# Kernel tuning notes

Hardware: AMD Instinct MI355X
Metric: run time of the kernel (lower is better)

The kernel has to match this reference:

```python
import jax, jax.numpy as jnp
import numpy as np

NUM_HEADS = 12
HEAD_DIM = 64
LOGIT_SCALE_MAX = 4.605170185988092  # log(1/0.01), open_clip default
EPS = 1e-12  # F.normalize eps


def setup_inputs() -> dict:
    key = jax.random.key(0)
    ks = jax.random.split(key, 8)
    N, L, C = 2, 2048, 768
    return {
        "x": jax.random.normal(ks[0], (N, L, C), dtype=jnp.float32),
        "in_proj_w": jax.random.normal(ks[1], (3 * C, C), dtype=jnp.float32) * 0.02,
        "in_proj_b": jax.random.normal(ks[2], (3 * C,), dtype=jnp.float32) * 0.02,
        "logit_scale": jax.random.normal(ks[3], (NUM_HEADS, 1, 1), dtype=jnp.float32),
        "learned_scale": jnp.ones((NUM_HEADS,), dtype=jnp.float32),
        "out_proj_w": jax.random.normal(ks[4], (C, C), dtype=jnp.float32) * 0.02,
        "out_proj_b": jax.random.normal(ks[5], (C,), dtype=jnp.float32) * 0.02,
        "attn_mask": jnp.zeros((L, L), dtype=jnp.float32),
    }


def _l2norm(t):
    # F.normalize(dim=-1): x / max(||x||, eps)
    n = jnp.linalg.norm(t, axis=-1, keepdims=True)
    return t / jnp.maximum(n, EPS)


def reference(x, in_proj_w, in_proj_b, logit_scale, learned_scale,
              out_proj_w, out_proj_b, attn_mask):
    N, L, C = x.shape
    H, D = NUM_HEADS, HEAD_DIM
    # packed QKV projection: [N, L, 3C]
    qkv = jnp.einsum("nlc,fc->nlf", x, in_proj_w) + in_proj_b
    q, k, v = jnp.split(qkv, 3, axis=-1)
    # [N, L, C] -> [N, H, L, D]
    to_heads = lambda t: t.reshape(N, L, H, D).transpose(0, 2, 1, 3)
    q, k, v = to_heads(q), to_heads(k), to_heads(v)
    # cosine attention with clamped exp logit scale per head
    attn = jnp.einsum("nhld,nhmd->nhlm", _l2norm(q), _l2norm(k))
    ls = jnp.exp(jnp.minimum(logit_scale, LOGIT_SCALE_MAX))  # [H,1,1]
    attn = attn * ls[None]  # broadcast over [N,H,L,L]
    attn = attn + attn_mask  # additive mask [L,L]
    attn = jax.nn.softmax(attn, axis=-1)
    out = jnp.einsum("nhlm,nhmd->nhld", attn, v)
    # learned per-head output scale
    out = out * learned_scale[None, :, None, None]
    # [N,H,L,D] -> [N,L,C]
    out = out.transpose(0, 2, 1, 3).reshape(N, L, C)
    out = jnp.einsum("nlc,fc->nlf", out, out_proj_w) + out_proj_b
    return out
```

## Files before the change

### kernel.cpp

```cpp
#include <hip/hip_runtime.h>
#include <math.h>

#define NB   2
#define SEQ  2048
#define CH   768
#define NH   12
#define HD   64
#define F3   2304
#define LSMAX 4.605170185988092f
#define LOG2E 1.4426950408889634f

typedef _Float16 f16;
typedef __attribute__((ext_vector_type(8))) _Float16 f16x8;
typedef __attribute__((ext_vector_type(4))) _Float16 f16x4;
typedef __attribute__((ext_vector_type(2))) _Float16 f16x2;
typedef __attribute__((ext_vector_type(4))) float f32x4;
typedef __attribute__((ext_vector_type(16))) float f32x16;

typedef __attribute__((address_space(3))) void lds_void;
typedef __attribute__((address_space(1))) const void gbl_cvoid;

#define QSZ   3145728
#define OATT  (3 * QSZ)
#define XHOFF 12582912
#define W1OFF 15728640
#define W2OFF 17498112
#define FLAGO 18087936

#define VCH   2048
#define VPLN  131072

#define GP2  72

#define KOFF(s, b) (((s) * 2 + (b)) * 2048)
#define VOFF(s, b) (8192 + ((s) * 2 + (b)) * 2304)

__global__ __launch_bounds__(256) void cvt_f16(const float* __restrict__ X,
                                               const float* __restrict__ W1,
                                               const float* __restrict__ W2,
                                               const float* __restrict__ M,
                                               f16* __restrict__ Xh,
                                               f16* __restrict__ W1h,
                                               f16* __restrict__ W2h,
                                               int* __restrict__ flag)
{
    int tid = blockIdx.x * 256 + threadIdx.x;
    if (blockIdx.y == 3) {
        if (tid < 1048576) {
            float4 v = ((const float4*)M)[tid];
            bool nz = (v.x != 0.f) || (v.y != 0.f) || (v.z != 0.f) || (v.w != 0.f);
            if (__any(nz) && (threadIdx.x & 63) == 0) atomicOr(flag, 1);
        }
        return;
    }
    const float* src; f16* dst; int n4;
    switch (blockIdx.y) {
        case 0:  src = X;  dst = Xh;  n4 = 786432;  break;
        case 1:  src = W1; dst = W1h; n4 = 442368;  break;
        default: src = W2; dst = W2h; n4 = 147456;  break;
    }
    if (tid < n4) {
        float4 v = ((const float4*)src)[tid];
        f16x4 o = {(f16)v.x, (f16)v.y, (f16)v.z, (f16)v.w};
        ((f16x4*)dst)[tid] = o;
    }
}

__global__ __launch_bounds__(256, 4) void qkv_gemm(const f16* __restrict__ Xh,
                                                   const f16* __restrict__ Wh,
                                                   const float* __restrict__ bias,
                                                   const float* __restrict__ logit_scale,
                                                   f16* __restrict__ qkv16)
{
    __shared__ f16 As[2][128 * 32];
    __shared__ f16 Bs[2][128 * 32];
    const int t    = threadIdx.x;
    const int w    = t >> 6;
    const int lane = t & 63;
    const int quad = lane >> 4;
    const int sub  = lane & 15;
    const int wm   = w & 1, wn = w >> 1;
    const int f0   = blockIdx.x * 128;
    const int m0   = blockIdx.y * 128;

    const int s0 = t, s1 = 256 + t;
    const int r0 = s0 >> 2, cb0 = ((s0 & 3) ^ (r0 & 3)) * 8;
    const int r1 = s1 >> 2, cb1 = ((s1 & 3) ^ (r1 & 3)) * 8;
    const f16* ga0 = Xh + (size_t)(m0 + r0) * CH + cb0;
    const f16* ga1 = Xh + (size_t)(m0 + r1) * CH + cb1;
    const f16* gb0 = Wh + (size_t)(f0 + r0) * CH + cb0;
    const f16* gb1 = Wh + (size_t)(f0 + r1) * CH + cb1;

    f32x4 acc[4][4];
#pragma unroll
    for (int i = 0; i < 4; ++i)
#pragma unroll
        for (int j = 0; j < 4; ++j) acc[i][j] = (f32x4){0.f, 0.f, 0.f, 0.f};

    const int pch = (quad ^ (sub & 3)) * 8;

    __builtin_amdgcn_global_load_lds((gbl_cvoid*)(ga0), (lds_void*)&As[0][s0 * 8], 16, 0, 0);
    __builtin_amdgcn_global_load_lds((gbl_cvoid*)(ga1), (lds_void*)&As[0][s1 * 8], 16, 0, 0);
    __builtin_amdgcn_global_load_lds((gbl_cvoid*)(gb0), (lds_void*)&Bs[0][s0 * 8], 16, 0, 0);
    __builtin_amdgcn_global_load_lds((gbl_cvoid*)(gb1), (lds_void*)&Bs[0][s1 * 8], 16, 0, 0);
    __syncthreads();

    for (int k0 = 0; k0 < CH; k0 += 32) {
        const int cur = (k0 >> 5) & 1, nxt = cur ^ 1;
        if (k0 + 32 < CH) {
            __builtin_amdgcn_global_load_lds((gbl_cvoid*)(ga0 + k0 + 32), (lds_void*)&As[nxt][s0 * 8], 16, 0, 0);
            __builtin_amdgcn_global_load_lds((gbl_cvoid*)(ga1 + k0 + 32), (lds_void*)&As[nxt][s1 * 8], 16, 0, 0);
            __builtin_amdgcn_global_load_lds((gbl_cvoid*)(gb0 + k0 + 32), (lds_void*)&Bs[nxt][s0 * 8], 16, 0, 0);
            __builtin_amdgcn_global_load_lds((gbl_cvoid*)(gb1 + k0 + 32), (lds_void*)&Bs[nxt][s1 * 8], 16, 0, 0);
        }
        f16x8 af[4], bf[4];
#pragma unroll
        for (int i = 0; i < 4; ++i) {
            af[i] = *(const f16x8*)&As[cur][(wm * 64 + i * 16 + sub) * 32 + pch];
            bf[i] = *(const f16x8*)&Bs[cur][(wn * 64 + i * 16 + sub) * 32 + pch];
        }
#pragma unroll
        for (int i = 0; i < 4; ++i)
#pragma unroll
            for (int j = 0; j < 4; ++j)
                acc[i][j] = __builtin_amdgcn_mfma_f32_16x16x32_f16(af[i], bf[j], acc[i][j], 0, 0, 0);
        __syncthreads();
    }

    const int t3 = f0 / CH;
    const int h  = ((f0 + wn * 64) % CH) >> 6;
    float bb[4];
#pragma unroll
    for (int j = 0; j < 4; ++j) bb[j] = bias[f0 + wn * 64 + j * 16 + sub];

    if (t3 == 2) {
        f16* vdst = qkv16 + (size_t)2 * QSZ;
#pragma unroll
        for (int i = 0; i < 4; ++i) {
            int mb = m0 + wm * 64 + i * 16 + quad * 4;
            int nn = mb >> 11, l0 = mb & 2047;
            f16* pl = vdst + (size_t)(nn * NH + h) * VPLN + (l0 >> 5) * VCH + (l0 & 31);
#pragma unroll
            for (int j = 0; j < 4; ++j) {
                f16x4 vv;
#pragma unroll
                for (int r = 0; r < 4; ++r) vv[r] = (f16)(acc[i][j][r] + bb[j]);
                *(f16x4*)(pl + (j * 16 + sub) * 32) = vv;
            }
        }
        return;
    }

    f16* dst = qkv16 + (size_t)t3 * QSZ;
    float lsv = (t3 == 0) ? __expf(fminf(logit_scale[h], LSMAX)) * LOG2E : 1.0f;
#pragma unroll
    for (int i = 0; i < 4; ++i) {
#pragma unroll
        for (int r = 0; r < 4; ++r) {
            int m = m0 + wm * 64 + i * 16 + quad * 4 + r;
            int n = m >> 11, l = m & 2047;
            float v[4];
#pragma unroll
            for (int j = 0; j < 4; ++j) v[j] = acc[i][j][r] + bb[j];
            float ss = v[0] * v[0] + v[1] * v[1] + v[2] * v[2] + v[3] * v[3];
#pragma unroll
            for (int mk = 1; mk < 16; mk <<= 1) ss += __shfl_xor(ss, mk, 64);
            float scale = 1.0f / fmaxf(sqrtf(ss), 1e-12f);
            if (t3 == 0) scale *= lsv;
            f16* drow = dst + (((size_t)n * NH + h) * SEQ + l) * HD;
#pragma unroll
            for (int j = 0; j < 4; ++j)
                drow[j * 16 + sub] = (f16)(v[j] * scale);
        }
    }
}

union V8 { f16x4 h[2]; f16x8 v; };
union U8 { int i[4]; f16x8 v; };

__device__ __forceinline__ void compute_chunk_lds(
    const f16* Kr, const f16* Vr, int rsw, int h2,
    const f16x8& qf0, const f16x8& qf1, const f16x8& qf2, const f16x8& qf3,
    int cc, bool has_mask, const float* __restrict__ Mg,
    f32x16& o0, f32x16& o1, float& m_run, float& l_acc)
{
    const f16x2 one2 = {(f16)1.f, (f16)1.f};
    f16x8 kf0 = *(const f16x8*)(Kr + ((8 * h2 + 0)  ^ rsw));
    f16x8 kf1 = *(const f16x8*)(Kr + ((8 * h2 + 16) ^ rsw));
    f16x8 kf2 = *(const f16x8*)(Kr + ((8 * h2 + 32) ^ rsw));
    f16x8 kf3 = *(const f16x8*)(Kr + ((8 * h2 + 48) ^ rsw));
    f32x16 sA = {};
    sA = __builtin_amdgcn_mfma_f32_32x32x16_f16(kf0, qf0, sA, 0, 0, 0);
    sA = __builtin_amdgcn_mfma_f32_32x32x16_f16(kf1, qf1, sA, 0, 0, 0);
    sA = __builtin_amdgcn_mfma_f32_32x32x16_f16(kf2, qf2, sA, 0, 0, 0);
    sA = __builtin_amdgcn_mfma_f32_32x32x16_f16(kf3, qf3, sA, 0, 0, 0);
    V8 va, vb, vc, vd;
    va.h[0] = *(const f16x4*)(Vr + 0);
    va.h[1] = *(const f16x4*)(Vr + 8);
    vb.h[0] = *(const f16x4*)(Vr + 16);
    vb.h[1] = *(const f16x4*)(Vr + 24);
    vc.h[0] = *(const f16x4*)(Vr + 1152 + 0);
    vc.h[1] = *(const f16x4*)(Vr + 1152 + 8);
    vd.h[0] = *(const f16x4*)(Vr + 1152 + 16);
    vd.h[1] = *(const f16x4*)(Vr + 1152 + 24);

    if (has_mask) {
#pragma unroll
        for (int rr = 0; rr < 16; ++rr) {
            int kk = cc * 32 + (rr & 3) + 8 * (rr >> 2) + 4 * h2;
            sA[rr] += LOG2E * Mg[kk];
        }
    }
    float mloc = sA[0];
#pragma unroll
    for (int rr = 1; rr < 16; ++rr) mloc = fmaxf(mloc, sA[rr]);
    float mfull = fmaxf(mloc, __shfl_xor(mloc, 32, 64));
    if (__any(mfull > m_run)) {
        float mnew = fmaxf(m_run, mfull);
        float al = exp2f(m_run - mnew);
        m_run = mnew;
        l_acc *= al;
#pragma unroll
        for (int rr = 0; rr < 16; ++rr) { o0[rr] *= al; o1[rr] *= al; }
    }
#pragma unroll
    for (int rr = 0; rr < 16; ++rr) sA[rr] = exp2f(sA[rr] - m_run);
#define PK(a, b) ({ f16x2 _t = {(f16)(a), (f16)(b)}; __builtin_bit_cast(int, _t); })
    U8 u0, u1;
    u0.i[0] = PK(sA[0], sA[1]);   u0.i[1] = PK(sA[2], sA[3]);
    u0.i[2] = PK(sA[4], sA[5]);   u0.i[3] = PK(sA[6], sA[7]);
    u1.i[0] = PK(sA[8], sA[9]);   u1.i[1] = PK(sA[10], sA[11]);
    u1.i[2] = PK(sA[12], sA[13]); u1.i[3] = PK(sA[14], sA[15]);
#undef PK
    l_acc = __builtin_amdgcn_fdot2(__builtin_bit_cast(f16x2, u0.i[0]), one2, l_acc, false);
    l_acc = __builtin_amdgcn_fdot2(__builtin_bit_cast(f16x2, u0.i[1]), one2, l_acc, false);
    l_acc = __builtin_amdgcn_fdot2(__builtin_bit_cast(f16x2, u0.i[2]), one2, l_acc, false);
    l_acc = __builtin_amdgcn_fdot2(__builtin_bit_cast(f16x2, u0.i[3]), one2, l_acc, false);
    l_acc = __builtin_amdgcn_fdot2(__builtin_bit_cast(f16x2, u1.i[0]), one2, l_acc, false);
    l_acc = __builtin_amdgcn_fdot2(__builtin_bit_cast(f16x2, u1.i[1]), one2, l_acc, false);
    l_acc = __builtin_amdgcn_fdot2(__builtin_bit_cast(f16x2, u1.i[2]), one2, l_acc, false);
    l_acc = __builtin_amdgcn_fdot2(__builtin_bit_cast(f16x2, u1.i[3]), one2, l_acc, false);
    o0 = __builtin_amdgcn_mfma_f32_32x32x16_f16(va.v, u0.v, o0, 0, 0, 0);
    o0 = __builtin_amdgcn_mfma_f32_32x32x16_f16(vb.v, u1.v, o0, 0, 0, 0);
    o1 = __builtin_amdgcn_mfma_f32_32x32x16_f16(vc.v, u0.v, o1, 0, 0, 0);
    o1 = __builtin_amdgcn_mfma_f32_32x32x16_f16(vd.v, u1.v, o1, 0, 0, 0);
}

__global__ __launch_bounds__(256, 3) void attn(const f16* __restrict__ Qh,
                                               const f16* __restrict__ Kh,
                                               const f16* __restrict__ Vt,
                                               const float* __restrict__ M32,
                                               const float* __restrict__ lscale,
                                               const int* __restrict__ flag,
                                               f16* __restrict__ Og)
{
    __shared__ f16x8 SMraw[2176];
    f16* SM = (f16*)SMraw;

    const int t    = threadIdx.x;
    const int w    = t >> 6;
    const int lane = t & 63;
    const int g    = w >> 1;
    const int s    = w & 1;
    const int r32  = lane & 31;
    const int h2   = lane >> 5;
    const int qb   = blockIdx.x * 64;
    const int hh   = blockIdx.y, n = blockIdx.z;
    const bool has_mask = (*flag) != 0;

    const int q = qb + g * 32 + r32;
    const f16* Qg  = Qh + ((size_t)(n * NH + hh) * SEQ + q) * HD + 8 * h2;
    const f16* KgH = Kh + ((size_t)(n * NH + hh) * SEQ + s * 1024) * HD;
    const f16* VgH = Vt + (size_t)(n * NH + hh) * VPLN + (size_t)(s * 32) * VCH;
    const float* Mg = M32 + (size_t)q * SEQ + s * 1024;

    f16x8 qf0 = *(const f16x8*)(Qg + 0);
    f16x8 qf1 = *(const f16x8*)(Qg + 16);
    f16x8 qf2 = *(const f16x8*)(Qg + 32);
    f16x8 qf3 = *(const f16x8*)(Qg + 48);

    const int th   = (g << 6) | lane;
    const int krow = th >> 2;
    const int kseg = (th & 3) << 4;
    const int ksw  = (krow & 7) << 3;
    const int vrow = th >> 1;
    const int vcol = (th & 1) << 4;
    const int rsw  = (r32 & 7) << 3;

    f16x8 kr0, kr1, vv0, vv1;
    {
        const f16* kp = KgH + krow * 64 + kseg;
        kr0 = *(const f16x8*)(kp);
        kr1 = *(const f16x8*)(kp + 8);
        const f16* vp = VgH + th * 16;
        vv0 = *(const f16x8*)(vp);
        vv1 = *(const f16x8*)(vp + 8);
        f16* Kw = SM + KOFF(s, 0) + krow * 64;
        f16* Vw = SM + VOFF(s, 0) + vrow * 36 + vcol;
        *(f16x8*)(Kw + ((kseg + 0) ^ ksw)) = kr0;
        *(f16x8*)(Kw + ((kseg + 8) ^ ksw)) = kr1;
        *(f16x8*)(Vw + 0) = vv0;
        *(f16x8*)(Vw + 8) = vv1;
    }
    __syncthreads();

    f32x16 o0 = {}, o1 = {};
    float m_run = -1e30f, l_acc = 0.f;

#pragma unroll 1
    for (int c = 0; c < 32; ++c) {
        const int buf = c & 1;
        if (c + 1 < 32) {
            const f16* kp = KgH + ((c + 1) * 32 + krow) * 64 + kseg;
            kr0 = *(const f16x8*)(kp);
            kr1 = *(const f16x8*)(kp + 8);
            const f16* vp = VgH + (c + 1) * VCH + th * 16;
            vv0 = *(const f16x8*)(vp);
            vv1 = *(const f16x8*)(vp + 8);
            __builtin_amdgcn_sched_barrier(0);
        }
        const f16* Kr = SM + KOFF(s, buf) + r32 * 64;
        const f16* Vr = SM + VOFF(s, buf) + r32 * 36 + 4 * h2;
        compute_chunk_lds(Kr, Vr, rsw, h2, qf0, qf1, qf2, qf3,
                          c, has_mask, Mg, o0, o1, m_run, l_acc);
        __syncthreads();
        if (c + 1 < 32) {
            const int nb = (c + 1) & 1;
            f16* Kw = SM + KOFF(s, nb) + krow * 64;
            f16* Vw = SM + VOFF(s, nb) + vrow * 36 + vcol;
            *(f16x8*)(Kw + ((kseg + 0) ^ ksw)) = kr0;
            *(f16x8*)(Kw + ((kseg + 8) ^ ksw)) = kr1;
            *(f16x8*)(Vw + 0) = vv0;
            *(f16x8*)(Vw + 8) = vv1;
            __syncthreads();
        }
    }

    float l_full = l_acc + __shfl_xor(l_acc, 32, 64);

    __syncthreads();
    float* OSp = (float*)SM;
    float* MSp = OSp + 4352;
    float* LSp = MSp + 64;

    if (s == 1) {
        if (h2 == 0) { MSp[g * 32 + r32] = m_run; LSp[g * 32 + r32] = l_full; }
#pragma unroll
        for (int rq = 0; rq < 4; ++rq) {
            int d0 = 8 * rq + 4 * h2;
            *(f32x4*)&OSp[(g * 32 + r32) * 68 + d0] =
                (f32x4){o0[rq * 4 + 0], o0[rq * 4 + 1], o0[rq * 4 + 2], o0[rq * 4 + 3]};
            *(f32x4*)&OSp[(g * 32 + r32) * 68 + d0 + 32] =
                (f32x4){o1[rq * 4 + 0], o1[rq * 4 + 1], o1[rq * 4 + 2], o1[rq * 4 + 3]};
        }
    }
    __syncthreads();
    if (s == 0) {
        float m_p = MSp[g * 32 + r32], l_p = LSp[g * 32 + r32];
        float mm = fmaxf(m_run, m_p);
        float a0 = exp2f(m_run - mm), a1 = exp2f(m_p - mm);
        float l_tot = a0 * l_full + a1 * l_p;
        float sc = lscale[hh] / l_tot;
        float sa = a0 * sc, sb = a1 * sc;
        f16* op = Og + ((size_t)n * SEQ + q) * CH + hh * 64;
#pragma unroll
        for (int rq = 0; rq < 4; ++rq) {
            int d0 = 8 * rq + 4 * h2;
            f32x4 p0 = *(const f32x4*)&OSp[(g * 32 + r32) * 68 + d0];
            f32x4 p1 = *(const f32x4*)&OSp[(g * 32 + r32) * 68 + d0 + 32];
            f16x4 ov0, ov1;
#pragma unroll
            for (int j = 0; j < 4; ++j) {
                ov0[j] = (f16)(o0[rq * 4 + j] * sa + p0[j] * sb);
                ov1[j] = (f16)(o1[rq * 4 + j] * sa + p1[j] * sb);
            }
            *(f16x4*)(op + d0)      = ov0;
            *(f16x4*)(op + 32 + d0) = ov1;
        }
    }
}

__global__ __launch_bounds__(256, 4) void out_gemm(const f16* __restrict__ A,
                                                   const f16* __restrict__ Wh,
                                                   const float* __restrict__ bias,
                                                   float* __restrict__ out)
{
    __shared__ f16 As[64 * GP2];
    __shared__ f16 Bs[64 * GP2];
    const int t    = threadIdx.x;
    const int w    = t >> 6;
    const int lane = t & 63;
    const int quad = lane >> 4;
    const int sub  = lane & 15;
    const int f0   = blockIdx.x * 64;
    const int m0   = blockIdx.y * 64;
    const int srow = t >> 2;
    const int sk   = (t & 3) * 16;

    const f16* ag = A + (size_t)(m0 + srow) * CH + sk;
    const f16* bg = Wh + (size_t)(f0 + srow) * CH + sk;
    f16x8 a0 = *(const f16x8*)(ag);
    f16x8 a1 = *(const f16x8*)(ag + 8);
    f16x8 b0 = *(const f16x8*)(bg);
    f16x8 b1 = *(const f16x8*)(bg + 8);

    f32x4 acc[4];
#pragma unroll
    for (int i = 0; i < 4; ++i) acc[i] = (f32x4){0.f, 0.f, 0.f, 0.f};

    for (int k0 = 0; k0 < CH; k0 += 64) {
        __syncthreads();
        *(f16x8*)&As[srow * GP2 + sk + 0] = a0;
        *(f16x8*)&As[srow * GP2 + sk + 8] = a1;
        *(f16x8*)&Bs[srow * GP2 + sk + 0] = b0;
        *(f16x8*)&Bs[srow * GP2 + sk + 8] = b1;
        __syncthreads();
        if (k0 + 64 < CH) {
            a0 = *(const f16x8*)(ag + k0 + 64);
            a1 = *(const f16x8*)(ag + k0 + 72);
            b0 = *(const f16x8*)(bg + k0 + 64);
            b1 = *(const f16x8*)(bg + k0 + 72);
        }
#pragma unroll
        for (int kk = 0; kk < 64; kk += 32) {
            f16x8 bf = *(const f16x8*)&Bs[(w * 16 + sub) * GP2 + kk + quad * 8];
#pragma unroll
            for (int i = 0; i < 4; ++i) {
                f16x8 af = *(const f16x8*)&As[(i * 16 + sub) * GP2 + kk + quad * 8];
                acc[i] = __builtin_amdgcn_mfma_f32_16x16x32_f16(af, bf, acc[i], 0, 0, 0);
            }
        }
    }
    float bb = bias[f0 + w * 16 + sub];
#pragma unroll
    for (int i = 0; i < 4; ++i)
#pragma unroll
        for (int r = 0; r < 4; ++r) {
            int m = m0 + i * 16 + quad * 4 + r;
            out[(size_t)m * CH + f0 + w * 16 + sub] = acc[i][r] + bb;
        }
}

extern "C" void kernel_launch(void* const* d_in, const int* in_sizes, int n_in,
                              void* d_out, int out_size, void* d_ws, size_t ws_size,
                              hipStream_t stream) {
    const float* x    = (const float*)d_in[0];
    const float* w1   = (const float*)d_in[1];
    const float* b1   = (const float*)d_in[2];
    const float* ls   = (const float*)d_in[3];
    const float* lrn  = (const float*)d_in[4];
    const float* w2   = (const float*)d_in[5];
    const float* b2   = (const float*)d_in[6];
    const float* msk  = (const float*)d_in[7];
    f16*   ws16 = (f16*)d_ws;
    int*   flag = (int*)(ws16 + FLAGO);
    float* out  = (float*)d_out;

    (void)hipMemsetAsync(flag, 0, 4, stream);
    hipLaunchKernelGGL(cvt_f16, dim3(4096, 4), dim3(256), 0, stream,
                       x, w1, w2, msk,
                       ws16 + XHOFF, ws16 + W1OFF, ws16 + W2OFF, flag);
    hipLaunchKernelGGL(qkv_gemm, dim3(F3 / 128, (NB * SEQ) / 128), dim3(256), 0, stream,
                       ws16 + XHOFF, ws16 + W1OFF, b1, ls, ws16);
    hipLaunchKernelGGL(attn, dim3(SEQ / 64, NH, NB), dim3(256), 0, stream,
                       ws16, ws16 + QSZ, ws16 + 2 * QSZ, msk, lrn, flag,
                       ws16 + OATT);
    hipLaunchKernelGGL(out_gemm, dim3(CH / 64, (NB * SEQ) / 64), dim3(256), 0, stream,
                       ws16 + OATT, ws16 + W2OFF, b2, out);
}
```

Baseline: 205.4 us.

## Unroll attention loop by two, skip small softmax rescales, use pkrtz conversion

The KV chunk loop is unrolled by two with fixed double-buffer pointers, so each pair of chunks needs one fewer workgroup barrier. The online-softmax rescale of the output accumulators is skipped unless the running max grows by more than 8 (log2 units), so exponentials can reach 256 before being stored as f16. The max reduction is written as a chain of 3-input max operations. The f16 packing switches to a single round-toward-zero pack conversion, which slightly changes rounding of the probabilities.

```diff
diff --git a/kernel.cpp b/kernel.cpp
--- a/kernel.cpp
+++ b/kernel.cpp
@@ -9,6 +9,7 @@
 #define F3   2304
 #define LSMAX 4.605170185988092f
 #define LOG2E 1.4426950408889634f
+#define RESCALE_THR 8.0f
 
 typedef _Float16 f16;
 typedef __attribute__((ext_vector_type(8))) _Float16 f16x8;
@@ -211,11 +212,16 @@
             sA[rr] += LOG2E * Mg[kk];
         }
     }
-    float mloc = sA[0];
-#pragma unroll
-    for (int rr = 1; rr < 16; ++rr) mloc = fmaxf(mloc, sA[rr]);
+    float m = fmaxf(fmaxf(sA[0], sA[1]), sA[2]);
+    m = fmaxf(fmaxf(m, sA[3]), sA[4]);
+    m = fmaxf(fmaxf(m, sA[5]), sA[6]);
+    m = fmaxf(fmaxf(m, sA[7]), sA[8]);
+    m = fmaxf(fmaxf(m, sA[9]), sA[10]);
+    m = fmaxf(fmaxf(m, sA[11]), sA[12]);
+    m = fmaxf(fmaxf(m, sA[13]), sA[14]);
+    float mloc = fmaxf(m, sA[15]);
     float mfull = fmaxf(mloc, __shfl_xor(mloc, 32, 64));
-    if (__any(mfull > m_run)) {
+    if (__any(mfull - m_run > RESCALE_THR)) {
         float mnew = fmaxf(m_run, mfull);
         float al = exp2f(m_run - mnew);
         m_run = mnew;
@@ -225,13 +231,15 @@
     }
 #pragma unroll
     for (int rr = 0; rr < 16; ++rr) sA[rr] = exp2f(sA[rr] - m_run);
-#define PK(a, b) ({ f16x2 _t = {(f16)(a), (f16)(b)}; __builtin_bit_cast(int, _t); })
     U8 u0, u1;
-    u0.i[0] = PK(sA[0], sA[1]);   u0.i[1] = PK(sA[2], sA[3]);
-    u0.i[2] = PK(sA[4], sA[5]);   u0.i[3] = PK(sA[6], sA[7]);
-    u1.i[0] = PK(sA[8], sA[9]);   u1.i[1] = PK(sA[10], sA[11]);
-    u1.i[2] = PK(sA[12], sA[13]); u1.i[3] = PK(sA[14], sA[15]);
-#undef PK
+    u0.i[0] = __builtin_bit_cast(int, __builtin_amdgcn_cvt_pkrtz(sA[0], sA[1]));
+    u0.i[1] = __builtin_bit_cast(int, __builtin_amdgcn_cvt_pkrtz(sA[2], sA[3]));
+    u0.i[2] = __builtin_bit_cast(int, __builtin_amdgcn_cvt_pkrtz(sA[4], sA[5]));
+    u0.i[3] = __builtin_bit_cast(int, __builtin_amdgcn_cvt_pkrtz(sA[6], sA[7]));
+    u1.i[0] = __builtin_bit_cast(int, __builtin_amdgcn_cvt_pkrtz(sA[8], sA[9]));
+    u1.i[1] = __builtin_bit_cast(int, __builtin_amdgcn_cvt_pkrtz(sA[10], sA[11]));
+    u1.i[2] = __builtin_bit_cast(int, __builtin_amdgcn_cvt_pkrtz(sA[12], sA[13]));
+    u1.i[3] = __builtin_bit_cast(int, __builtin_amdgcn_cvt_pkrtz(sA[14], sA[15]));
     l_acc = __builtin_amdgcn_fdot2(__builtin_bit_cast(f16x2, u0.i[0]), one2, l_acc, false);
     l_acc = __builtin_amdgcn_fdot2(__builtin_bit_cast(f16x2, u0.i[1]), one2, l_acc, false);
     l_acc = __builtin_amdgcn_fdot2(__builtin_bit_cast(f16x2, u0.i[2]), one2, l_acc, false);
@@ -287,6 +295,15 @@
     const int vcol = (th & 1) << 4;
     const int rsw  = (r32 & 7) << 3;
 
+    f16* Kw0 = SM + KOFF(s, 0) + krow * 64;
+    f16* Kw1 = SM + KOFF(s, 1) + krow * 64;
+    f16* Vw0 = SM + VOFF(s, 0) + vrow * 36 + vcol;
+    f16* Vw1 = SM + VOFF(s, 1) + vrow * 36 + vcol;
+    const f16* Kr0 = SM + KOFF(s, 0) + r32 * 64;
+    const f16* Kr1 = SM + KOFF(s, 1) + r32 * 64;
+    const f16* Vr0 = SM + VOFF(s, 0) + r32 * 36 + 4 * h2;
+    const f16* Vr1 = SM + VOFF(s, 1) + r32 * 36 + 4 * h2;
+
     f16x8 kr0, kr1, vv0, vv1;
     {
         const f16* kp = KgH + krow * 64 + kseg;
@@ -295,12 +312,10 @@
         const f16* vp = VgH + th * 16;
         vv0 = *(const f16x8*)(vp);
         vv1 = *(const f16x8*)(vp + 8);
-        f16* Kw = SM + KOFF(s, 0) + krow * 64;
-        f16* Vw = SM + VOFF(s, 0) + vrow * 36 + vcol;
-        *(f16x8*)(Kw + ((kseg + 0) ^ ksw)) = kr0;
-        *(f16x8*)(Kw + ((kseg + 8) ^ ksw)) = kr1;
-        *(f16x8*)(Vw + 0) = vv0;
-        *(f16x8*)(Vw + 8) = vv1;
+        *(f16x8*)(Kw0 + ((kseg + 0) ^ ksw)) = kr0;
+        *(f16x8*)(Kw0 + ((kseg + 8) ^ ksw)) = kr1;
+        *(f16x8*)(Vw0 + 0) = vv0;
+        *(f16x8*)(Vw0 + 8) = vv1;
     }
     __syncthreads();
 
@@ -308,9 +323,8 @@
     float m_run = -1e30f, l_acc = 0.f;
 
 #pragma unroll 1
-    for (int c = 0; c < 32; ++c) {
-        const int buf = c & 1;
-        if (c + 1 < 32) {
+    for (int c = 0; c < 32; c += 2) {
+        {
             const f16* kp = KgH + ((c + 1) * 32 + krow) * 64 + kseg;
             kr0 = *(const f16x8*)(kp);
             kr1 = *(const f16x8*)(kp + 8);
@@ -319,19 +333,29 @@
             vv1 = *(const f16x8*)(vp + 8);
             __builtin_amdgcn_sched_barrier(0);
         }
-        const f16* Kr = SM + KOFF(s, buf) + r32 * 64;
-        const f16* Vr = SM + VOFF(s, buf) + r32 * 36 + 4 * h2;
-        compute_chunk_lds(Kr, Vr, rsw, h2, qf0, qf1, qf2, qf3,
+        compute_chunk_lds(Kr0, Vr0, rsw, h2, qf0, qf1, qf2, qf3,
                           c, has_mask, Mg, o0, o1, m_run, l_acc);
+        *(f16x8*)(Kw1 + ((kseg + 0) ^ ksw)) = kr0;
+        *(f16x8*)(Kw1 + ((kseg + 8) ^ ksw)) = kr1;
+        *(f16x8*)(Vw1 + 0) = vv0;
+        *(f16x8*)(Vw1 + 8) = vv1;
         __syncthreads();
-        if (c + 1 < 32) {
-            const int nb = (c + 1) & 1;
-            f16* Kw = SM + KOFF(s, nb) + krow * 64;
-            f16* Vw = SM + VOFF(s, nb) + vrow * 36 + vcol;
-            *(f16x8*)(Kw + ((kseg + 0) ^ ksw)) = kr0;
-            *(f16x8*)(Kw + ((kseg + 8) ^ ksw)) = kr1;
-            *(f16x8*)(Vw + 0) = vv0;
-            *(f16x8*)(Vw + 8) = vv1;
+        if (c + 2 < 32) {
+            const f16* kp = KgH + ((c + 2) * 32 + krow) * 64 + kseg;
+            kr0 = *(const f16x8*)(kp);
+            kr1 = *(const f16x8*)(kp + 8);
+            const f16* vp = VgH + (c + 2) * VCH + th * 16;
+            vv0 = *(const f16x8*)(vp);
+            vv1 = *(const f16x8*)(vp + 8);
+            __builtin_amdgcn_sched_barrier(0);
+        }
+        compute_chunk_lds(Kr1, Vr1, rsw, h2, qf0, qf1, qf2, qf3,
+                          c + 1, has_mask, Mg, o0, o1, m_run, l_acc);
+        if (c + 2 < 32) {
+            *(f16x8*)(Kw0 + ((kseg + 0) ^ ksw)) = kr0;
+            *(f16x8*)(Kw0 + ((kseg + 8) ^ ksw)) = kr1;
+            *(f16x8*)(Vw0 + 0) = vv0;
+            *(f16x8*)(Vw0 + 8) = vv1;
             __syncthreads();
         }
     }
```

Result: faster. 195.4 us (-4.9%).
